# Kernel tuning notes

Hardware: AMD Instinct MI355X
Metric: run time of the kernel (lower is better)

The kernel has to match this reference:

```python
import jax, jax.numpy as jnp
import numpy as np
import math

N_EMBD = 64
HEAD_SIZE = 64
B, T = 16, 2048


def setup_inputs() -> dict:
    key = jax.random.key(0)
    k1, k2, k3, k4 = jax.random.split(key, 4)
    inputs = jax.random.normal(k1, (B, T, N_EMBD), dtype=jnp.float32)
    # Causal mask: True where attention is NOT allowed (upper triangle),
    # matching masked_fill_(mask, -1e9) with mask = ~tril.
    mask = jnp.triu(jnp.ones((T, T), dtype=bool), k=1)
    # nn.Linear(n_embd, head_size, bias=False) weights, stored as
    # (n_embd, head_size) so projection is inputs @ W (== x @ W_torch.T).
    scale = 1.0 / math.sqrt(N_EMBD)
    Wq = jax.random.uniform(k2, (N_EMBD, HEAD_SIZE), jnp.float32, -scale, scale)
    Wk = jax.random.uniform(k3, (N_EMBD, HEAD_SIZE), jnp.float32, -scale, scale)
    Wv = jax.random.uniform(k4, (N_EMBD, HEAD_SIZE), jnp.float32, -scale, scale)
    return {"inputs": inputs, "mask": mask, "Wq": Wq, "Wk": Wk, "Wv": Wv}


def reference(inputs, mask, Wq, Wk, Wv):
    # inputs: (B, T, n_embd); mask: (T, T) bool broadcast over batch
    q = inputs @ Wq  # (B, T, H)
    k = inputs @ Wk  # (B, T, H)
    v = inputs @ Wv  # (B, T, H)
    inv_sqrt_h = 1.0 / math.sqrt(HEAD_SIZE)
    scores = jnp.einsum('bth,bsh->bts', q, k) * inv_sqrt_h  # (B, T, T)
    scores = jnp.where(mask, jnp.float32(-1e9), scores)
    attention = jax.nn.softmax(scores, axis=-1)
    out = jnp.einsum('bts,bsh->bth', attention, v)  # (B, T, H)
    return out
```

## Files before the change

### kernel.cpp

```cpp
#include <hip/hip_runtime.h>
#include <stdint.h>


typedef __bf16 bf16x8 __attribute__((ext_vector_type(8)));
typedef __bf16 bf16x4 __attribute__((ext_vector_type(4)));
typedef float f32x4 __attribute__((ext_vector_type(4)));

#define QSCALE 0.18033688011112042f
#define MFMA16(a, b, c) __builtin_amdgcn_mfma_f32_16x16x32_bf16((a), (b), (c), 0, 0, 0)

__device__ __forceinline__ unsigned short f2bf(float f) {
  union { float f; unsigned u; } x; x.f = f;
  unsigned r = x.u + 0x7fffu + ((x.u >> 16) & 1u);
  return (unsigned short)(r >> 16);
}

__device__ __forceinline__ int swz(int row, int bytecol) {
  return row * 128 + (bytecol ^ ((row & 7) << 4));
}
__device__ __forceinline__ bf16x8 frag(const unsigned short* base, int row, int kf, int lane) {
  int off = swz(row, kf * 64 + ((lane >> 4) << 4));
  return *(const bf16x8*)((const char*)base + off);
}

__global__ __launch_bounds__(256, 2) void proj_kernel(
    const float* __restrict__ X, const float* __restrict__ Wq,
    const float* __restrict__ Wk, const float* __restrict__ Wv,
    unsigned short* __restrict__ Qg, unsigned short* __restrict__ Kg,
    unsigned short* __restrict__ Vtg) {
  __shared__ __align__(16) unsigned short Xs[256 * 64];
  __shared__ __align__(16) unsigned short Ws[3 * 64 * 64];
  const int tid = threadIdx.x, lane = tid & 63, w = tid >> 6;
  const int ln = lane & 15, g = lane >> 4;
  const long grow0 = (long)blockIdx.x * 256;
  const int b = (int)(grow0 >> 11);
  const int tin0 = (int)(grow0 & 2047);

#pragma unroll
  for (int pass = 0; pass < 4; ++pass) {
    const int r = pass * 64 + (tid >> 2), c = tid & 3;
    const float* src = X + (grow0 + r) * 64 + c * 16;
    float4 f0 = *(const float4*)src;
    float4 f1 = *(const float4*)(src + 4);
    float4 f2 = *(const float4*)(src + 8);
    float4 f3 = *(const float4*)(src + 12);
    uint4 d0, d1;
    d0.x = f2bf(f0.x) | ((unsigned)f2bf(f0.y) << 16);
    d0.y = f2bf(f0.z) | ((unsigned)f2bf(f0.w) << 16);
    d0.z = f2bf(f1.x) | ((unsigned)f2bf(f1.y) << 16);
    d0.w = f2bf(f1.z) | ((unsigned)f2bf(f1.w) << 16);
    d1.x = f2bf(f2.x) | ((unsigned)f2bf(f2.y) << 16);
    d1.y = f2bf(f2.z) | ((unsigned)f2bf(f2.w) << 16);
    d1.z = f2bf(f3.x) | ((unsigned)f2bf(f3.y) << 16);
    d1.w = f2bf(f3.z) | ((unsigned)f2bf(f3.w) << 16);
    *(uint4*)((char*)Xs + swz(r, c * 32)) = d0;
    *(uint4*)((char*)Xs + swz(r, c * 32 + 16)) = d1;
  }
  for (int c = tid; c < 3 * 4096; c += 256) {
    const int mat = c >> 12, rr = c & 4095;
    const int e = rr >> 6, hh = rr & 63;
    const float* wsrc = (mat == 0) ? Wq : (mat == 1) ? Wk : Wv;
    *(unsigned short*)((char*)(Ws + mat * 4096) + swz(hh, e * 2)) = f2bf(wsrc[rr]);
  }
  __syncthreads();

  const f32x4 zero = {0.f, 0.f, 0.f, 0.f};
  const int rbase = w * 64;

#pragma unroll
  for (int s = 0; s < 4; ++s) {
    const int xrow = rbase + s * 16;
    bf16x8 a0 = frag(Xs, xrow + ln, 0, lane);
    bf16x8 a1 = frag(Xs, xrow + ln, 1, lane);
#pragma unroll
    for (int mat = 0; mat < 2; ++mat) {
      unsigned short* dst = mat ? Kg : Qg;
      const unsigned short* wbase = Ws + mat * 4096;
#pragma unroll
      for (int nt = 0; nt < 4; ++nt) {
        bf16x8 b0 = frag(wbase, nt * 16 + ln, 0, lane);
        bf16x8 b1 = frag(wbase, nt * 16 + ln, 1, lane);
        f32x4 acc = MFMA16(a0, b0, zero);
        acc = MFMA16(a1, b1, acc);
        long row0 = grow0 + xrow + g * 4;
        int col = nt * 16 + ln;
#pragma unroll
        for (int k = 0; k < 4; ++k) {
          float v = acc[k];
          if (mat == 0) v *= QSCALE;
          dst[(row0 + k) * 64 + col] = f2bf(v);
        }
      }
    }
    const unsigned short* wv = Ws + 2 * 4096;
    bf16x8 xb0 = a0, xb1 = a1;
#pragma unroll
    for (int mt = 0; mt < 4; ++mt) {
      bf16x8 wa0 = frag(wv, mt * 16 + ln, 0, lane);
      bf16x8 wa1 = frag(wv, mt * 16 + ln, 1, lane);
      f32x4 acc = MFMA16(wa0, xb0, zero);
      acc = MFMA16(wa1, xb1, acc);
      int t = tin0 + xrow + ln;
      int h0 = mt * 16 + g * 4;
#pragma unroll
      for (int k = 0; k < 4; ++k)
        Vtg[((long)(b * 64 + h0 + k)) * 2048 + t] = f2bf(acc[k]);
    }
  }
}

__global__ __launch_bounds__(256, 2) void attn5_kernel(
    const unsigned short* __restrict__ Qg, const unsigned short* __restrict__ Kg,
    const unsigned short* __restrict__ Vtg, float* __restrict__ Og) {
  __shared__ __align__(16) unsigned char smem[35840];

  const int bid = blockIdx.x;
  const int slot = bid >> 3;
  const int b = ((bid & 7) << 1) + (slot & 1);
  const int m = slot >> 1;
  const int qt = (slot & 1) ? (31 - m) : m;
  const int q0 = qt * 64;
  const int ns = qt + 1;

  const int tid = threadIdx.x;
  const int lane = tid & 63, w = tid >> 6;
  const int g = lane >> 4, ln = lane & 15;
  const int h = w & 1, qh = w >> 1;

  const unsigned short* qrow = Qg + ((long)b * 2048 + q0 + qh * 32) * 64;
  const bf16x8 qb00 = *(const bf16x8*)(qrow + ln * 64 + g * 8);
  const bf16x8 qb01 = *(const bf16x8*)(qrow + ln * 64 + 32 + g * 8);
  const bf16x8 qb10 = *(const bf16x8*)(qrow + (16 + ln) * 64 + g * 8);
  const bf16x8 qb11 = *(const bf16x8*)(qrow + (16 + ln) * 64 + 32 + g * 8);

  const unsigned short* kbase = Kg + (long)b * 2048 * 64;
  const unsigned short* vbase = Vtg + (long)b * 64 * 2048;

  const int sr = tid >> 2;
  const int sc = tid & 3;

  const f32x4 zero = {0.f, 0.f, 0.f, 0.f};
  f32x4 o0[4], o1[4];
#pragma unroll
  for (int nt = 0; nt < 4; ++nt) { o0[nt] = zero; o1[nt] = zero; }
  float den0 = 0.f, den1 = 0.f;

  {
    const unsigned short* kg = kbase + (long)sr * 64 + sc * 16;
    uint4 k0 = *(const uint4*)kg;
    uint4 k1 = *(const uint4*)(kg + 8);
    const unsigned short* vg = vbase + (long)sr * 2048 + sc * 16;
    uint4 v0 = *(const uint4*)vg;
    uint4 v1 = *(const uint4*)(vg + 8);
    unsigned short* Kb = (unsigned short*)smem;
    unsigned short* Vb = (unsigned short*)(smem + 8192);
    *(uint4*)((char*)Kb + swz(sr, sc * 32)) = k0;
    *(uint4*)((char*)Kb + swz(sr, sc * 32 + 16)) = k1;
    *(uint4*)((char*)Vb + swz(sr, sc * 32)) = v0;
    *(uint4*)((char*)Vb + swz(sr, sc * 32 + 16)) = v1;
  }
  __syncthreads();

  int cur = 0;
  for (int t = 0; t < ns; ++t) {
    const int kv0 = t * 64;
    const bool pre = (t + 1 < ns);
    uint4 k0, k1, v0, v1;
    if (pre) {
      const int kv0n = kv0 + 64;
      const unsigned short* kg = kbase + (long)(kv0n + sr) * 64 + sc * 16;
      k0 = *(const uint4*)kg;
      k1 = *(const uint4*)(kg + 8);
      const unsigned short* vg = vbase + (long)sr * 2048 + kv0n + sc * 16;
      v0 = *(const uint4*)vg;
      v1 = *(const uint4*)(vg + 8);
    }

    const unsigned short* Kb = (const unsigned short*)(smem + cur * 16384);
    const unsigned short* Vb = (const unsigned short*)(smem + cur * 16384 + 8192);

    bf16x8 ka00 = frag(Kb, h * 32 + ln,      0, lane);
    bf16x8 ka01 = frag(Kb, h * 32 + ln,      1, lane);
    bf16x8 ka10 = frag(Kb, h * 32 + 16 + ln, 0, lane);
    bf16x8 ka11 = frag(Kb, h * 32 + 16 + ln, 1, lane);

    bf16x8 vb[4];
#pragma unroll
    for (int nt = 0; nt < 4; ++nt) {
      int row = nt * 16 + ln;
      bf16x4 lo = *(const bf16x4*)((const char*)Vb + swz(row, h * 64 + g * 8));
      bf16x4 hi = *(const bf16x4*)((const char*)Vb + swz(row, h * 64 + 32 + g * 8));
      vb[nt] = __builtin_shufflevector(lo, hi, 0, 1, 2, 3, 4, 5, 6, 7);
    }

    __builtin_amdgcn_s_setprio(1);
    f32x4 st00 = MFMA16(ka00, qb00, zero);  st00 = MFMA16(ka01, qb01, st00);
    f32x4 st01 = MFMA16(ka00, qb10, zero);  st01 = MFMA16(ka01, qb11, st01);
    f32x4 st10 = MFMA16(ka10, qb00, zero);  st10 = MFMA16(ka11, qb01, st10);
    f32x4 st11 = MFMA16(ka10, qb10, zero);  st11 = MFMA16(ka11, qb11, st11);
    __builtin_amdgcn_s_setprio(0);

    if (t == ns - 1) {
      const int qg0 = q0 + qh * 32 + ln;
      const int qg1 = qg0 + 16;
      const int kvb = kv0 + h * 32 + g * 4;
#pragma unroll
      for (int i = 0; i < 4; ++i) {
        if (kvb + i > qg0)      st00[i] = -1e30f;
        if (kvb + i > qg1)      st01[i] = -1e30f;
        if (kvb + 16 + i > qg0) st10[i] = -1e30f;
        if (kvb + 16 + i > qg1) st11[i] = -1e30f;
      }
    }

    bf16x8 pa0, pa1;
#pragma unroll
    for (int i = 0; i < 4; ++i) {
      float p00 = exp2f(st00[i]);
      float p10 = exp2f(st10[i]);
      float p01 = exp2f(st01[i]);
      float p11 = exp2f(st11[i]);
      den0 += p00 + p10;
      den1 += p01 + p11;
      pa0[i] = (__bf16)p00;  pa0[4 + i] = (__bf16)p10;
      pa1[i] = (__bf16)p01;  pa1[4 + i] = (__bf16)p11;
    }

    __builtin_amdgcn_s_setprio(1);
#pragma unroll
    for (int nt = 0; nt < 4; ++nt) {
      o0[nt] = MFMA16(pa0, vb[nt], o0[nt]);
      o1[nt] = MFMA16(pa1, vb[nt], o1[nt]);
    }
    __builtin_amdgcn_s_setprio(0);

    if (pre) {
      unsigned short* Kn = (unsigned short*)(smem + (cur ^ 1) * 16384);
      unsigned short* Vn = (unsigned short*)(smem + (cur ^ 1) * 16384 + 8192);
      *(uint4*)((char*)Kn + swz(sr, sc * 32)) = k0;
      *(uint4*)((char*)Kn + swz(sr, sc * 32 + 16)) = k1;
      *(uint4*)((char*)Vn + swz(sr, sc * 32)) = v0;
      *(uint4*)((char*)Vn + swz(sr, sc * 32 + 16)) = v1;
    }
    __syncthreads();
    cur ^= 1;
  }

  den0 += __shfl_xor(den0, 16);
  den0 += __shfl_xor(den0, 32);
  den1 += __shfl_xor(den1, 16);
  den1 += __shfl_xor(den1, 32);

  float* Olds = (float*)smem;
  float* Dlds = (float*)(smem + 34816);
#pragma unroll
  for (int nt = 0; nt < 4; ++nt)
#pragma unroll
    for (int i = 0; i < 4; ++i) {
      Olds[(h * 64 + qh * 32 + g * 4 + i) * 68 + nt * 16 + ln] = o0[nt][i];
      Olds[(h * 64 + qh * 32 + 16 + g * 4 + i) * 68 + nt * 16 + ln] = o1[nt][i];
    }
  if (lane < 16) {
    Dlds[h * 64 + qh * 32 + ln] = den0;
    Dlds[h * 64 + qh * 32 + 16 + ln] = den1;
  }
  __syncthreads();

  const int q = tid >> 2;
  const int d0 = (tid & 3) * 16;
  float dd = Dlds[q] + Dlds[64 + q];
  float inv = 1.0f / dd;
  float acc[16];
#pragma unroll
  for (int e = 0; e < 16; ++e)
    acc[e] = (Olds[q * 68 + d0 + e] + Olds[(64 + q) * 68 + d0 + e]) * inv;
  float* outp = Og + ((long)b * 2048 + q0 + q) * 64 + d0;
#pragma unroll
  for (int v4 = 0; v4 < 4; ++v4)
    *(float4*)(outp + v4 * 4) = make_float4(acc[v4 * 4], acc[v4 * 4 + 1],
                                            acc[v4 * 4 + 2], acc[v4 * 4 + 3]);
}

extern "C" void kernel_launch(void* const* d_in, const int* in_sizes, int n_in,
                              void* d_out, int out_size, void* d_ws, size_t ws_size,
                              hipStream_t stream) {
  const float* X  = (const float*)d_in[0];
  const float* Wq = (const float*)d_in[2];
  const float* Wk = (const float*)d_in[3];
  const float* Wv = (const float*)d_in[4];

  unsigned short* Qg  = (unsigned short*)d_ws;
  unsigned short* Kg  = Qg + 2097152;
  unsigned short* Vtg = Kg + 2097152;

  proj_kernel<<<128, 256, 0, stream>>>(X, Wq, Wk, Wv, Qg, Kg, Vtg);
  attn5_kernel<<<512, 256, 0, stream>>>(Qg, Kg, Vtg, (float*)d_out);
}
```

Before: 50.06 us.

## Split projection into more blocks and pre-transpose weights in a prep kernel

New measurement: 50.77 us. Within noise of the previous version (+1.4%).

```diff
diff --git a/kernel.cpp b/kernel.cpp
--- a/kernel.cpp
+++ b/kernel.cpp
@@ -23,22 +23,31 @@
   return *(const bf16x8*)((const char*)base + off);
 }
 
+__global__ void prep_w_kernel(const float* __restrict__ Wq, const float* __restrict__ Wk,
+                              const float* __restrict__ Wv, unsigned short* __restrict__ WT) {
+  int mat = blockIdx.x;
+  const float* src = (mat == 0) ? Wq : (mat == 1) ? Wk : Wv;
+  unsigned short* dst = WT + mat * 4096;
+  for (int idx = threadIdx.x; idx < 4096; idx += 256) {
+    int e = idx >> 6, h = idx & 63;
+    dst[h * 64 + e] = f2bf(src[e * 64 + h]);
+  }
+}
+
 __global__ __launch_bounds__(256, 2) void proj_kernel(
-    const float* __restrict__ X, const float* __restrict__ Wq,
-    const float* __restrict__ Wk, const float* __restrict__ Wv,
+    const float* __restrict__ X, const unsigned short* __restrict__ WT,
     unsigned short* __restrict__ Qg, unsigned short* __restrict__ Kg,
     unsigned short* __restrict__ Vtg) {
-  __shared__ __align__(16) unsigned short Xs[256 * 64];
+  __shared__ __align__(16) unsigned short Xs[64 * 64];
   __shared__ __align__(16) unsigned short Ws[3 * 64 * 64];
   const int tid = threadIdx.x, lane = tid & 63, w = tid >> 6;
   const int ln = lane & 15, g = lane >> 4;
-  const long grow0 = (long)blockIdx.x * 256;
+  const long grow0 = (long)blockIdx.x * 64;
   const int b = (int)(grow0 >> 11);
   const int tin0 = (int)(grow0 & 2047);
 
-#pragma unroll
-  for (int pass = 0; pass < 4; ++pass) {
-    const int r = pass * 64 + (tid >> 2), c = tid & 3;
+  {
+    const int r = tid >> 2, c = tid & 3;
     const float* src = X + (grow0 + r) * 64 + c * 16;
     float4 f0 = *(const float4*)src;
     float4 f1 = *(const float4*)(src + 4);
@@ -56,33 +65,31 @@
     *(uint4*)((char*)Xs + swz(r, c * 32)) = d0;
     *(uint4*)((char*)Xs + swz(r, c * 32 + 16)) = d1;
   }
-  for (int c = tid; c < 3 * 4096; c += 256) {
-    const int mat = c >> 12, rr = c & 4095;
-    const int e = rr >> 6, hh = rr & 63;
-    const float* wsrc = (mat == 0) ? Wq : (mat == 1) ? Wk : Wv;
-    *(unsigned short*)((char*)(Ws + mat * 4096) + swz(hh, e * 2)) = f2bf(wsrc[rr]);
+  for (int c = tid; c < 1536; c += 256) {
+    int mat = c >> 9, cc = c & 511;
+    int r = cc >> 3, k = cc & 7;
+    uint4 d = *(const uint4*)(WT + mat * 4096 + r * 64 + k * 8);
+    *(uint4*)((char*)(Ws + mat * 4096) + swz(r, k * 16)) = d;
   }
   __syncthreads();
 
   const f32x4 zero = {0.f, 0.f, 0.f, 0.f};
-  const int rbase = w * 64;
-
-#pragma unroll
-  for (int s = 0; s < 4; ++s) {
-    const int xrow = rbase + s * 16;
-    bf16x8 a0 = frag(Xs, xrow + ln, 0, lane);
-    bf16x8 a1 = frag(Xs, xrow + ln, 1, lane);
-#pragma unroll
-    for (int mat = 0; mat < 2; ++mat) {
+#pragma unroll
+  for (int i = 0; i < 3; ++i) {
+    const int task = w * 3 + i;
+    const int mat = task >> 2, s = task & 3;
+    const unsigned short* wbase = Ws + mat * 4096;
+    if (mat < 2) {
+      bf16x8 a0 = frag(Xs, s * 16 + ln, 0, lane);
+      bf16x8 a1 = frag(Xs, s * 16 + ln, 1, lane);
       unsigned short* dst = mat ? Kg : Qg;
-      const unsigned short* wbase = Ws + mat * 4096;
 #pragma unroll
       for (int nt = 0; nt < 4; ++nt) {
         bf16x8 b0 = frag(wbase, nt * 16 + ln, 0, lane);
         bf16x8 b1 = frag(wbase, nt * 16 + ln, 1, lane);
         f32x4 acc = MFMA16(a0, b0, zero);
         acc = MFMA16(a1, b1, acc);
-        long row0 = grow0 + xrow + g * 4;
+        long row0 = grow0 + s * 16 + g * 4;
         int col = nt * 16 + ln;
 #pragma unroll
         for (int k = 0; k < 4; ++k) {
@@ -91,20 +98,21 @@
           dst[(row0 + k) * 64 + col] = f2bf(v);
         }
       }
-    }
-    const unsigned short* wv = Ws + 2 * 4096;
-    bf16x8 xb0 = a0, xb1 = a1;
-#pragma unroll
-    for (int mt = 0; mt < 4; ++mt) {
-      bf16x8 wa0 = frag(wv, mt * 16 + ln, 0, lane);
-      bf16x8 wa1 = frag(wv, mt * 16 + ln, 1, lane);
-      f32x4 acc = MFMA16(wa0, xb0, zero);
-      acc = MFMA16(wa1, xb1, acc);
-      int t = tin0 + xrow + ln;
-      int h0 = mt * 16 + g * 4;
-#pragma unroll
-      for (int k = 0; k < 4; ++k)
-        Vtg[((long)(b * 64 + h0 + k)) * 2048 + t] = f2bf(acc[k]);
+    } else {
+      bf16x8 a0 = frag(wbase, s * 16 + ln, 0, lane);
+      bf16x8 a1 = frag(wbase, s * 16 + ln, 1, lane);
+#pragma unroll
+      for (int nt = 0; nt < 4; ++nt) {
+        bf16x8 b0 = frag(Xs, nt * 16 + ln, 0, lane);
+        bf16x8 b1 = frag(Xs, nt * 16 + ln, 1, lane);
+        f32x4 acc = MFMA16(a0, b0, zero);
+        acc = MFMA16(a1, b1, acc);
+        int t = tin0 + nt * 16 + ln;
+        int h0 = s * 16 + g * 4;
+#pragma unroll
+        for (int k = 0; k < 4; ++k)
+          Vtg[((long)(b * 64 + h0 + k)) * 2048 + t] = f2bf(acc[k]);
+      }
     }
   }
 }
@@ -292,7 +300,9 @@
   unsigned short* Qg  = (unsigned short*)d_ws;
   unsigned short* Kg  = Qg + 2097152;
   unsigned short* Vtg = Kg + 2097152;
-
-  proj_kernel<<<128, 256, 0, stream>>>(X, Wq, Wk, Wv, Qg, Kg, Vtg);
+  unsigned short* WT  = Vtg + 2097152;
+
+  prep_w_kernel<<<3, 256, 0, stream>>>(Wq, Wk, Wv, WT);
+  proj_kernel<<<512, 256, 0, stream>>>(X, WT, Qg, Kg, Vtg);
   attn5_kernel<<<512, 256, 0, stream>>>(Qg, Kg, Vtg, (float*)d_out);
 }
```

## Shrink projection blocks to 64 rows and vectorize Q/K/V stores

Applied to the files above, without the earlier changes.

New measurement: 50.95 us. No clear change (+1.8%).

```diff
diff --git a/kernel.cpp b/kernel.cpp
--- a/kernel.cpp
+++ b/kernel.cpp
@@ -28,17 +28,16 @@
     const float* __restrict__ Wk, const float* __restrict__ Wv,
     unsigned short* __restrict__ Qg, unsigned short* __restrict__ Kg,
     unsigned short* __restrict__ Vtg) {
-  __shared__ __align__(16) unsigned short Xs[256 * 64];
+  __shared__ __align__(16) unsigned short Xs[64 * 64];
   __shared__ __align__(16) unsigned short Ws[3 * 64 * 64];
   const int tid = threadIdx.x, lane = tid & 63, w = tid >> 6;
   const int ln = lane & 15, g = lane >> 4;
-  const long grow0 = (long)blockIdx.x * 256;
+  const long grow0 = (long)blockIdx.x * 64;
   const int b = (int)(grow0 >> 11);
   const int tin0 = (int)(grow0 & 2047);
 
-#pragma unroll
-  for (int pass = 0; pass < 4; ++pass) {
-    const int r = pass * 64 + (tid >> 2), c = tid & 3;
+  {
+    const int r = tid >> 2, c = tid & 3;
     const float* src = X + (grow0 + r) * 64 + c * 16;
     float4 f0 = *(const float4*)src;
     float4 f1 = *(const float4*)(src + 4);
@@ -65,46 +64,45 @@
   __syncthreads();
 
   const f32x4 zero = {0.f, 0.f, 0.f, 0.f};
-  const int rbase = w * 64;
-
-#pragma unroll
-  for (int s = 0; s < 4; ++s) {
-    const int xrow = rbase + s * 16;
-    bf16x8 a0 = frag(Xs, xrow + ln, 0, lane);
-    bf16x8 a1 = frag(Xs, xrow + ln, 1, lane);
-#pragma unroll
-    for (int mat = 0; mat < 2; ++mat) {
+#pragma unroll
+  for (int i = 0; i < 3; ++i) {
+    const int task = w * 3 + i;
+    const int mat = task >> 2, s = task & 3;
+    bf16x8 x0 = frag(Xs, s * 16 + ln, 0, lane);
+    bf16x8 x1 = frag(Xs, s * 16 + ln, 1, lane);
+    if (mat < 2) {
       unsigned short* dst = mat ? Kg : Qg;
       const unsigned short* wbase = Ws + mat * 4096;
-#pragma unroll
-      for (int nt = 0; nt < 4; ++nt) {
-        bf16x8 b0 = frag(wbase, nt * 16 + ln, 0, lane);
-        bf16x8 b1 = frag(wbase, nt * 16 + ln, 1, lane);
-        f32x4 acc = MFMA16(a0, b0, zero);
-        acc = MFMA16(a1, b1, acc);
-        long row0 = grow0 + xrow + g * 4;
-        int col = nt * 16 + ln;
-#pragma unroll
-        for (int k = 0; k < 4; ++k) {
-          float v = acc[k];
-          if (mat == 0) v *= QSCALE;
-          dst[(row0 + k) * 64 + col] = f2bf(v);
+      const long trow = grow0 + s * 16 + ln;
+#pragma unroll
+      for (int mt = 0; mt < 4; ++mt) {
+        bf16x8 wa0 = frag(wbase, mt * 16 + ln, 0, lane);
+        bf16x8 wa1 = frag(wbase, mt * 16 + ln, 1, lane);
+        f32x4 acc = MFMA16(wa0, x0, zero);
+        acc = MFMA16(wa1, x1, acc);
+        if (mat == 0) {
+#pragma unroll
+          for (int k = 0; k < 4; ++k) acc[k] *= QSCALE;
         }
+        uint2 pk;
+        pk.x = f2bf(acc[0]) | ((unsigned)f2bf(acc[1]) << 16);
+        pk.y = f2bf(acc[2]) | ((unsigned)f2bf(acc[3]) << 16);
+        *(uint2*)(dst + trow * 64 + mt * 16 + g * 4) = pk;
       }
-    }
-    const unsigned short* wv = Ws + 2 * 4096;
-    bf16x8 xb0 = a0, xb1 = a1;
-#pragma unroll
-    for (int mt = 0; mt < 4; ++mt) {
-      bf16x8 wa0 = frag(wv, mt * 16 + ln, 0, lane);
-      bf16x8 wa1 = frag(wv, mt * 16 + ln, 1, lane);
-      f32x4 acc = MFMA16(wa0, xb0, zero);
-      acc = MFMA16(wa1, xb1, acc);
-      int t = tin0 + xrow + ln;
-      int h0 = mt * 16 + g * 4;
-#pragma unroll
-      for (int k = 0; k < 4; ++k)
-        Vtg[((long)(b * 64 + h0 + k)) * 2048 + t] = f2bf(acc[k]);
+    } else {
+      const unsigned short* wv = Ws + 2 * 4096;
+      const int t0 = tin0 + s * 16 + g * 4;
+#pragma unroll
+      for (int mt = 0; mt < 4; ++mt) {
+        bf16x8 wb0 = frag(wv, mt * 16 + ln, 0, lane);
+        bf16x8 wb1 = frag(wv, mt * 16 + ln, 1, lane);
+        f32x4 acc = MFMA16(x0, wb0, zero);
+        acc = MFMA16(x1, wb1, acc);
+        uint2 pk;
+        pk.x = f2bf(acc[0]) | ((unsigned)f2bf(acc[1]) << 16);
+        pk.y = f2bf(acc[2]) | ((unsigned)f2bf(acc[3]) << 16);
+        *(uint2*)(Vtg + ((long)(b * 64 + mt * 16 + ln)) * 2048 + t0) = pk;
+      }
     }
   }
 }
@@ -293,6 +291,6 @@
   unsigned short* Kg  = Qg + 2097152;
   unsigned short* Vtg = Kg + 2097152;
 
-  proj_kernel<<<128, 256, 0, stream>>>(X, Wq, Wk, Wv, Qg, Kg, Vtg);
+  proj_kernel<<<512, 256, 0, stream>>>(X, Wq, Wk, Wv, Qg, Kg, Vtg);
   attn5_kernel<<<512, 256, 0, stream>>>(Qg, Kg, Vtg, (float*)d_out);
 }
```
